# Performance work log

Measured on AMD Instinct MI355X. Metric: run time of the kernel, lower is better.

Reference implementation:

```python
import jax, jax.numpy as jnp
import numpy as np

B, S, D, H = 2, 2048, 1024, 16
HD = D // H  # head_dim = 64


def setup_inputs() -> dict:
    key = jax.random.key(0)
    ks = jax.random.split(key, 10)
    s = 1.0 / np.sqrt(D)
    # causal mask: 0 on/below diagonal, -inf above (matches masked_fill(mask == -inf))
    neg_inf = jnp.float32(-jnp.inf)
    mask = jnp.where(jnp.tril(jnp.ones((S, S), dtype=bool)), 0.0, neg_inf).astype(jnp.float32)
    return {
        "x": jax.random.normal(ks[0], (B, S, D), dtype=jnp.float32),
        "mask": mask,
        "Wq": jax.random.uniform(ks[1], (D, D), jnp.float32, -s, s),
        "bq": jax.random.uniform(ks[2], (D,), jnp.float32, -s, s),
        "Wk": jax.random.uniform(ks[3], (D, D), jnp.float32, -s, s),
        "bk": jax.random.uniform(ks[4], (D,), jnp.float32, -s, s),
        "Wv": jax.random.uniform(ks[5], (D, D), jnp.float32, -s, s),
        "bv": jax.random.uniform(ks[6], (D,), jnp.float32, -s, s),
        "Wo": jax.random.uniform(ks[7], (D, D), jnp.float32, -s, s),
        "bo": jax.random.uniform(ks[8], (D,), jnp.float32, -s, s),
    }


def reference(x, mask, Wq, bq, Wk, bk, Wv, bv, Wo, bo):
    b, s, d = x.shape
    scale = jnp.float32(HD) ** 0.5
    # qkv projections (torch Linear: y = x W^T + b), split into heads: [b, H, s, hd]
    q = (x @ Wq.T + bq).reshape(b, s, H, HD).transpose(0, 2, 1, 3)
    k = (x @ Wk.T + bk).reshape(b, s, H, HD).transpose(0, 2, 1, 3)
    v = (x @ Wv.T + bv).reshape(b, s, H, HD).transpose(0, 2, 1, 3)
    scores = jnp.einsum("bhqd,bhkd->bhqk", q, k) / scale
    scores = jnp.where(mask[None, None] == -jnp.inf, -jnp.inf, scores)
    attn = jax.nn.softmax(scores, axis=-1)
    # dropout(p=0.1) is identity in eval mode
    ctx = jnp.einsum("bhqk,bhkd->bhqd", attn, v)
    ctx = ctx.transpose(0, 2, 1, 3).reshape(b, s, d)
    return ctx @ Wo.T + bo
```

## Files before the change

### kernel.cpp

```cpp
#include <hip/hip_runtime.h>
#include <hip/hip_bf16.h>
#include <cmath>

#define S_ 2048
#define D_ 1024
#define H_ 16
#define HD_ 64
#define GM 4096
#define GN 1024
#define GK 1024
#define QSCALE 0.1803368801111f
#define THR2   11.5415603f

typedef __attribute__((ext_vector_type(4))) float f32x4;
typedef __attribute__((ext_vector_type(8))) short bf16x8;
typedef __attribute__((ext_vector_type(4))) short bf16x4;

__device__ __forceinline__ short f2bf(float f) {
    union { float f; unsigned u; } x; x.f = f;
    unsigned r = x.u + 0x7fffu + ((x.u >> 16) & 1u);
    return (short)(r >> 16);
}
__device__ __forceinline__ short bftrunc(float f) {
    union { float f; unsigned u; } x; x.f = f;
    return (short)(x.u >> 16);
}
__device__ __forceinline__ void gload16(const short* g, short* l) {
    __builtin_amdgcn_global_load_lds((const __attribute__((address_space(1))) void*)g,
                                     (__attribute__((address_space(3))) void*)l, 16, 0, 0);
}

__global__ __launch_bounds__(256) void cvt_all(
    const float* __restrict__ x,
    const float* __restrict__ w0, const float* __restrict__ w1,
    const float* __restrict__ w2, const float* __restrict__ w3,
    short* __restrict__ xb, short* __restrict__ Wb)
{
    const int bid = blockIdx.x;
    const float* src; short* dst; int loc;
    if (bid < 2048) { src = x; dst = xb; loc = bid; }
    else {
        int wsel = (bid - 2048) >> 9, wb = (bid - 2048) & 511;
        src = wsel == 0 ? w0 : wsel == 1 ? w1 : wsel == 2 ? w2 : w3;
        dst = Wb + ((size_t)wsel << 20);
        loc = wb;
    }
    int id = loc * 256 + threadIdx.x;
    const float* s = src + (size_t)id * 8;
    f32x4 a = *(const f32x4*)s;
    f32x4 b = *(const f32x4*)(s + 4);
    bf16x8 h;
    h[0] = f2bf(a[0]); h[1] = f2bf(a[1]); h[2] = f2bf(a[2]); h[3] = f2bf(a[3]);
    h[4] = f2bf(b[0]); h[5] = f2bf(b[1]); h[6] = f2bf(b[2]); h[7] = f2bf(b[3]);
    *(bf16x8*)(dst + (size_t)id * 8) = h;
}

__global__ __launch_bounds__(256) void gemm_qkv(
    const short* __restrict__ A, const short* __restrict__ W3,
    const float* __restrict__ bq, const float* __restrict__ bk, const float* __restrict__ bv,
    short* __restrict__ Qb, short* __restrict__ Kb, short* __restrict__ Vt)
{
    __shared__ short SMEM[32768];
    const int t = threadIdx.x, lane = t & 63, w = t >> 6;
    const int bid = blockIdx.x;
    const int xcd = bid & 7, idx = bid >> 3;
    const int ntile = idx % 24, mloc = idx / 24;
    const int m0 = (xcd * 4 + mloc) * 128;
    const int n0g = ntile * 128;
    const int wr = (w >> 1) * 64, wc = (w & 1) * 64;
    const int fr = lane & 15, g = lane >> 4;
    const int srow = lane >> 3;
    const int gslot = (lane & 7) ^ srow;
    const int rbase = w * 32;

    f32x4 acc[4][4] = {};

    #pragma unroll
    for (int i = 0; i < 4; ++i) {
        int row = rbase + i * 8 + srow;
        gload16(A  + (size_t)(m0 + row) * GK + gslot * 8, &SMEM[(rbase + i * 8) * 64]);
        gload16(W3 + (size_t)(n0g + row) * GK + gslot * 8, &SMEM[8192 + (rbase + i * 8) * 64]);
    }
    __syncthreads();

    int cur = 0;
    for (int t16 = 0; t16 < 16; ++t16) {
        if (t16 < 15) {
            int kt = (t16 + 1) * 64;
            short* Ad = &SMEM[(cur ^ 1) * 16384];
            short* Bd = &SMEM[(cur ^ 1) * 16384 + 8192];
            #pragma unroll
            for (int i = 0; i < 4; ++i) {
                int row = rbase + i * 8 + srow;
                gload16(A  + (size_t)(m0 + row) * GK + kt + gslot * 8, &Ad[(rbase + i * 8) * 64]);
                gload16(W3 + (size_t)(n0g + row) * GK + kt + gslot * 8, &Bd[(rbase + i * 8) * 64]);
            }
        }
        const char* Asc = (const char*)&SMEM[cur * 16384];
        const char* Bsc = (const char*)&SMEM[cur * 16384 + 8192];
        #pragma unroll
        for (int ks = 0; ks < 2; ++ks) {
            bf16x8 af[4], bf_[4];
            #pragma unroll
            for (int mb = 0; mb < 4; ++mb) {
                int row = wr + mb * 16 + fr;
                af[mb] = *(const bf16x8*)(Asc + row * 128 + (((ks * 4 + g) ^ (row & 7)) << 4));
            }
            #pragma unroll
            for (int nb = 0; nb < 4; ++nb) {
                int row = wc + nb * 16 + fr;
                bf_[nb] = *(const bf16x8*)(Bsc + row * 128 + (((ks * 4 + g) ^ (row & 7)) << 4));
            }
            #pragma unroll
            for (int mb = 0; mb < 4; ++mb)
                #pragma unroll
                for (int nb = 0; nb < 4; ++nb)
                    acc[mb][nb] = __builtin_amdgcn_mfma_f32_16x16x32_bf16(
                        af[mb], bf_[nb], acc[mb][nb], 0, 0, 0);
        }
        __syncthreads();
        cur ^= 1;
    }

    const int seg = n0g >> 10, nn = n0g & 1023;
    if (seg == 2) {
        short* Cs = SMEM;
        #pragma unroll
        for (int mb = 0; mb < 4; ++mb)
            #pragma unroll
            for (int nb = 0; nb < 4; ++nb) {
                int cl = wc + nb * 16 + fr;
                int rl_ = wr + mb * 16 + g * 4;
                float bvv = bv[nn + cl];
                bf16x4 hv;
                #pragma unroll
                for (int r = 0; r < 4; ++r) hv[r] = f2bf(acc[mb][nb][r] + bvv);
                *(bf16x4*)(Cs + cl * 136 + rl_) = hv;
            }
        __syncthreads();
        const int b = m0 >> 11;
        const int s_base = m0 & 2047;
        #pragma unroll
        for (int p = 0; p < 8; ++p) {
            int id = t + p * 256;
            int cl = id >> 4, ch = id & 15;
            int n = nn + cl;
            int h = n >> 6, d = n & 63;
            bf16x8 v = *(const bf16x8*)(Cs + cl * 136 + ch * 8);
            *(bf16x8*)(Vt + ((size_t)((b * 16 + h) * 64 + d)) * S_ + s_base + ch * 8) = v;
        }
    } else {
        const float* bp = seg ? bk : bq;
        short* dst = seg ? Kb : Qb;
        const float sc = seg ? 1.0f : QSCALE;
        #pragma unroll
        for (int mb = 0; mb < 4; ++mb)
            #pragma unroll
            for (int nb = 0; nb < 4; ++nb) {
                int grow = m0 + wr + mb * 16 + g * 4;
                int gcol = nn + wc + nb * 16 + fr;
                float bvv = bp[gcol];
                #pragma unroll
                for (int r = 0; r < 4; ++r)
                    dst[(size_t)(grow + r) * GN + gcol] = f2bf((acc[mb][nb][r] + bvv) * sc);
            }
    }
}

__global__ __launch_bounds__(256) void gemm_o(
    const short* __restrict__ A, const short* __restrict__ W,
    const float* __restrict__ bias, float* __restrict__ C)
{
    __shared__ short As[2][8192];
    __shared__ short Bs[2][4096];
    const int t = threadIdx.x, lane = t & 63, w = t >> 6;
    const int bid = blockIdx.x;
    const int xcd = bid & 7, wk = bid >> 3;
    const int m0 = (xcd * 4 + (wk & 3)) * 128;
    const int n0 = (wk >> 2) * 64;
    const int wr = (w >> 1) * 64, wc = (w & 1) * 32;
    const int fr = lane & 15, g = lane >> 4;
    const int srow = lane >> 3;
    const int gslot = (lane & 7) ^ srow;
    const int rbase = w * 32;
    const int brow = w * 16;

    f32x4 acc[4][2] = {};

    #pragma unroll
    for (int i = 0; i < 4; ++i) {
        int row = rbase + i * 8 + srow;
        gload16(A + (size_t)(m0 + row) * GK + gslot * 8, &As[0][(rbase + i * 8) * 64]);
    }
    #pragma unroll
    for (int i = 0; i < 2; ++i) {
        int row = brow + i * 8 + srow;
        gload16(W + (size_t)(n0 + row) * GK + gslot * 8, &Bs[0][(brow + i * 8) * 64]);
    }
    __syncthreads();

    int cur = 0;
    for (int t64 = 0; t64 < 16; ++t64) {
        if (t64 < 15) {
            int kt = (t64 + 1) * 64;
            #pragma unroll
            for (int i = 0; i < 4; ++i) {
                int row = rbase + i * 8 + srow;
                gload16(A + (size_t)(m0 + row) * GK + kt + gslot * 8, &As[cur ^ 1][(rbase + i * 8) * 64]);
            }
            #pragma unroll
            for (int i = 0; i < 2; ++i) {
                int row = brow + i * 8 + srow;
                gload16(W + (size_t)(n0 + row) * GK + kt + gslot * 8, &Bs[cur ^ 1][(brow + i * 8) * 64]);
            }
        }
        #pragma unroll
        for (int ks = 0; ks < 2; ++ks) {
            bf16x8 af[4], bf_[2];
            #pragma unroll
            for (int mb = 0; mb < 4; ++mb) {
                int row = wr + mb * 16 + fr;
                af[mb] = *(const bf16x8*)((const char*)&As[cur][0] + row * 128 + (((ks * 4 + g) ^ (row & 7)) << 4));
            }
            #pragma unroll
            for (int nb = 0; nb < 2; ++nb) {
                int row = wc + nb * 16 + fr;
                bf_[nb] = *(const bf16x8*)((const char*)&Bs[cur][0] + row * 128 + (((ks * 4 + g) ^ (row & 7)) << 4));
            }
            #pragma unroll
            for (int mb = 0; mb < 4; ++mb)
                #pragma unroll
                for (int nb = 0; nb < 2; ++nb)
                    acc[mb][nb] = __builtin_amdgcn_mfma_f32_16x16x32_bf16(
                        af[mb], bf_[nb], acc[mb][nb], 0, 0, 0);
        }
        __syncthreads();
        cur ^= 1;
    }

    #pragma unroll
    for (int mb = 0; mb < 4; ++mb)
        #pragma unroll
        for (int nb = 0; nb < 2; ++nb) {
            int grow = m0 + wr + mb * 16 + g * 4;
            int gcol = n0 + wc + nb * 16 + fr;
            float bvv = bias[gcol];
            #pragma unroll
            for (int r = 0; r < 4; ++r)
                C[(size_t)(grow + r) * GN + gcol] = acc[mb][nb][r] + bvv;
        }
}

__global__ __launch_bounds__(256) void attn_fwd_bf16(
    const short* __restrict__ Qb, const short* __restrict__ Kb,
    const short* __restrict__ Vtb, short* __restrict__ Ob)
{
    __shared__ short SK[2][4096];
    __shared__ short SVT[2][4096];
    __shared__ short SP[4][1024];

    const int t = threadIdx.x, lane = t & 63, w = t >> 6;
    const int g = lane >> 4, fr = lane & 15;
    const int bid = blockIdx.x;
    const int xcd = bid & 7, idx = bid >> 3;
    const int bh = xcd * 4 + (idx & 3);
    const int qt = 31 - (idx >> 2);
    const int b = bh >> 4, h = bh & 15;
    const int q0 = qt * 64;
    const int wq0 = w * 16;
    const int nt = qt + 1;

    bf16x8 qf[2];
    #pragma unroll
    for (int ks = 0; ks < 2; ++ks)
        qf[ks] = *(const bf16x8*)(Qb + (size_t)(b * S_ + q0 + wq0 + fr) * D_
                                  + h * 64 + ks * 32 + g * 8);

    const int srow8 = lane >> 3;
    const short* kp[2];
    const short* vp[2];
    short* kd0[2]; short* kd1[2]; short* vd0[2]; short* vd1[2];
    #pragma unroll
    for (int i = 0; i < 2; ++i) {
        int row = w * 16 + i * 8 + srow8;
        int gsl = (lane & 7) ^ (row & 7);
        kp[i] = Kb + (size_t)(b * S_ + row) * D_ + h * 64 + gsl * 8;
        vp[i] = Vtb + (size_t)(bh * 64 + row) * S_ + gsl * 8;
        kd0[i] = &SK[0][(w * 16 + i * 8) * 64];  kd1[i] = &SK[1][(w * 16 + i * 8) * 64];
        vd0[i] = &SVT[0][(w * 16 + i * 8) * 64]; vd1[i] = &SVT[1][(w * 16 + i * 8) * 64];
    }
    short* SPw = &SP[w][0];
    const int qsw = fr & 7;

    #pragma unroll
    for (int i = 0; i < 2; ++i) {
        gload16(kp[i], kd0[i]);
        gload16(vp[i], vd0[i]);
    }
    __syncthreads();

    f32x4 Oacc[4] = {};
    float m2 = -1e30f, lsum = 0.f;
    int cur = 0;

    for (int kt = 0; kt < nt; ++kt) {
        if (kt + 1 < nt) {
            kp[0] += 64 * D_; kp[1] += 64 * D_;
            vp[0] += 64;      vp[1] += 64;
            if (cur) {
                #pragma unroll
                for (int i = 0; i < 2; ++i) { gload16(kp[i], kd0[i]); gload16(vp[i], vd0[i]); }
            } else {
                #pragma unroll
                for (int i = 0; i < 2; ++i) { gload16(kp[i], kd1[i]); gload16(vp[i], vd1[i]); }
            }
        }
        const char* SKc = (const char*)(cur ? &SK[1][0] : &SK[0][0]);
        const char* SVc = (const char*)(cur ? &SVT[1][0] : &SVT[0][0]);

        f32x4 sacc[4] = {};
        #pragma unroll
        for (int ks = 0; ks < 2; ++ks) {
            #pragma unroll
            for (int mk = 0; mk < 4; ++mk) {
                int row = mk * 16 + fr;
                bf16x8 kf = *(const bf16x8*)(SKc + row * 128 + (((ks * 4 + g) ^ (row & 7)) << 4));
                sacc[mk] = __builtin_amdgcn_mfma_f32_16x16x32_bf16(kf, qf[ks], sacc[mk], 0, 0, 0);
            }
        }
        if (kt == qt) {
            #pragma unroll
            for (int mk = 0; mk < 4; ++mk)
                #pragma unroll
                for (int r = 0; r < 4; ++r)
                    if (mk * 16 + g * 4 + r > wq0 + fr) sacc[mk][r] = -1e30f;
        }

        float mx[4];
        #pragma unroll
        for (int mk = 0; mk < 4; ++mk)
            mx[mk] = fmaxf(fmaxf(sacc[mk][0], sacc[mk][1]), fmaxf(sacc[mk][2], sacc[mk][3]));
        float rm = fmaxf(fmaxf(mx[0], mx[1]), fmaxf(mx[2], mx[3]));
        rm = fmaxf(rm, __shfl_xor(rm, 16));
        rm = fmaxf(rm, __shfl_xor(rm, 32));
        if (rm > m2 + THR2) {
            float resc = exp2f(m2 - rm);
            m2 = rm;
            lsum *= resc;
            #pragma unroll
            for (int md = 0; md < 4; ++md)
                #pragma unroll
                for (int r = 0; r < 4; ++r) Oacc[md][r] *= resc;
        }
        float psk[4];
        #pragma unroll
        for (int mk = 0; mk < 4; ++mk) {
            float p0 = exp2f(sacc[mk][0] - m2);
            float p1 = exp2f(sacc[mk][1] - m2);
            float p2 = exp2f(sacc[mk][2] - m2);
            float p3 = exp2f(sacc[mk][3] - m2);
            psk[mk] = (p0 + p1) + (p2 + p3);
            bf16x4 pk;
            pk[0] = bftrunc(p0); pk[1] = bftrunc(p1);
            pk[2] = bftrunc(p2); pk[3] = bftrunc(p3);
            int k = mk * 16 + g * 4;
            *(bf16x4*)((char*)SPw + fr * 128 + (((k >> 3) ^ qsw) << 4) + ((k & 7) << 1)) = pk;
        }
        float ps = (psk[0] + psk[1]) + (psk[2] + psk[3]);
        ps += __shfl_xor(ps, 16);
        ps += __shfl_xor(ps, 32);
        lsum += ps;

        #pragma unroll
        for (int ks = 0; ks < 2; ++ks) {
            bf16x8 pf = *(const bf16x8*)((const char*)SPw + fr * 128 + (((ks * 4 + g) ^ qsw) << 4));
            #pragma unroll
            for (int md = 0; md < 4; ++md) {
                int row = md * 16 + fr;
                bf16x8 vf = *(const bf16x8*)(SVc + row * 128 + (((ks * 4 + g) ^ (row & 7)) << 4));
                Oacc[md] = __builtin_amdgcn_mfma_f32_16x16x32_bf16(vf, pf, Oacc[md], 0, 0, 0);
            }
        }
        __syncthreads();
        cur ^= 1;
    }

    const float rl = 1.f / lsum;
    const size_t orow = (size_t)(b * S_ + q0 + wq0 + fr) * D_ + h * 64;
    #pragma unroll
    for (int md = 0; md < 4; ++md) {
        bf16x4 ov;
        #pragma unroll
        for (int r = 0; r < 4; ++r) ov[r] = f2bf(Oacc[md][r] * rl);
        *(bf16x4*)(Ob + orow + md * 16 + g * 4) = ov;
    }
}

extern "C" void kernel_launch(void* const* d_in, const int* in_sizes, int n_in,
                              void* d_out, int out_size, void* d_ws, size_t ws_size,
                              hipStream_t stream)
{
    const float* x  = (const float*)d_in[0];
    const float* Wq = (const float*)d_in[2];
    const float* bq = (const float*)d_in[3];
    const float* Wk = (const float*)d_in[4];
    const float* bk = (const float*)d_in[5];
    const float* Wv = (const float*)d_in[6];
    const float* bv = (const float*)d_in[7];
    const float* Wo = (const float*)d_in[8];
    const float* bo = (const float*)d_in[9];
    float* out = (float*)d_out;

    const size_t MD = (size_t)GM * D_;
    short* xb = (short*)d_ws;
    short* Wb = xb + MD;
    short* Qb = Wb + 4 * (size_t)D_ * D_;
    short* Kb = Qb + MD;
    short* Vt = Kb + MD;
    short* Ob = Vt + MD;

    dim3 blk(256);
    cvt_all<<<dim3(4096), blk, 0, stream>>>(x, Wq, Wk, Wv, Wo, xb, Wb);
    gemm_qkv<<<dim3(768), blk, 0, stream>>>(xb, Wb, bq, bk, bv, Qb, Kb, Vt);
    attn_fwd_bf16<<<dim3(1024), blk, 0, stream>>>(Qb, Kb, Vt, Ob);
    gemm_o<<<dim3(512), blk, 0, stream>>>(Ob, Wb + 3 * (size_t)D_ * D_, bo, out);
}
```

Measured before the change: 113.3 us.

## Use two warps per attention block, each handling 32 query rows

```diff
diff --git a/kernel.cpp b/kernel.cpp
--- a/kernel.cpp
+++ b/kernel.cpp
@@ -251,13 +251,13 @@
         }
 }
 
-__global__ __launch_bounds__(256) void attn_fwd_bf16(
+__global__ __launch_bounds__(128) void attn_fwd_bf16(
     const short* __restrict__ Qb, const short* __restrict__ Kb,
     const short* __restrict__ Vtb, short* __restrict__ Ob)
 {
     __shared__ short SK[2][4096];
     __shared__ short SVT[2][4096];
-    __shared__ short SP[4][1024];
+    __shared__ short SP[2][2048];
 
     const int t = threadIdx.x, lane = t & 63, w = t >> 6;
     const int g = lane >> 4, fr = lane & 15;
@@ -267,132 +267,163 @@
     const int qt = 31 - (idx >> 2);
     const int b = bh >> 4, h = bh & 15;
     const int q0 = qt * 64;
-    const int wq0 = w * 16;
+    const int wq0 = w * 32;
     const int nt = qt + 1;
 
-    bf16x8 qf[2];
-    #pragma unroll
-    for (int ks = 0; ks < 2; ++ks)
-        qf[ks] = *(const bf16x8*)(Qb + (size_t)(b * S_ + q0 + wq0 + fr) * D_
-                                  + h * 64 + ks * 32 + g * 8);
+    bf16x8 qf[2][2];
+    #pragma unroll
+    for (int nq = 0; nq < 2; ++nq)
+        #pragma unroll
+        for (int ks = 0; ks < 2; ++ks)
+            qf[nq][ks] = *(const bf16x8*)(Qb + (size_t)(b * S_ + q0 + wq0 + nq * 16 + fr) * D_
+                                          + h * 64 + ks * 32 + g * 8);
 
     const int srow8 = lane >> 3;
-    const short* kp[2];
-    const short* vp[2];
-    short* kd0[2]; short* kd1[2]; short* vd0[2]; short* vd1[2];
-    #pragma unroll
-    for (int i = 0; i < 2; ++i) {
-        int row = w * 16 + i * 8 + srow8;
+    const short* kp[4];
+    const short* vp[4];
+    short* kd0[4]; short* kd1[4]; short* vd0[4]; short* vd1[4];
+    #pragma unroll
+    for (int i = 0; i < 4; ++i) {
+        int row = w * 32 + i * 8 + srow8;
         int gsl = (lane & 7) ^ (row & 7);
         kp[i] = Kb + (size_t)(b * S_ + row) * D_ + h * 64 + gsl * 8;
         vp[i] = Vtb + (size_t)(bh * 64 + row) * S_ + gsl * 8;
-        kd0[i] = &SK[0][(w * 16 + i * 8) * 64];  kd1[i] = &SK[1][(w * 16 + i * 8) * 64];
-        vd0[i] = &SVT[0][(w * 16 + i * 8) * 64]; vd1[i] = &SVT[1][(w * 16 + i * 8) * 64];
+        kd0[i] = &SK[0][(w * 32 + i * 8) * 64];  kd1[i] = &SK[1][(w * 32 + i * 8) * 64];
+        vd0[i] = &SVT[0][(w * 32 + i * 8) * 64]; vd1[i] = &SVT[1][(w * 32 + i * 8) * 64];
     }
     short* SPw = &SP[w][0];
     const int qsw = fr & 7;
 
     #pragma unroll
-    for (int i = 0; i < 2; ++i) {
+    for (int i = 0; i < 4; ++i) {
         gload16(kp[i], kd0[i]);
         gload16(vp[i], vd0[i]);
     }
     __syncthreads();
 
-    f32x4 Oacc[4] = {};
-    float m2 = -1e30f, lsum = 0.f;
+    f32x4 Oacc[2][4] = {};
+    float m2[2] = { -1e30f, -1e30f };
+    float lsum[2] = { 0.f, 0.f };
     int cur = 0;
 
     for (int kt = 0; kt < nt; ++kt) {
         if (kt + 1 < nt) {
-            kp[0] += 64 * D_; kp[1] += 64 * D_;
-            vp[0] += 64;      vp[1] += 64;
+            #pragma unroll
+            for (int i = 0; i < 4; ++i) { kp[i] += 64 * D_; vp[i] += 64; }
             if (cur) {
                 #pragma unroll
-                for (int i = 0; i < 2; ++i) { gload16(kp[i], kd0[i]); gload16(vp[i], vd0[i]); }
+                for (int i = 0; i < 4; ++i) { gload16(kp[i], kd0[i]); gload16(vp[i], vd0[i]); }
             } else {
                 #pragma unroll
-                for (int i = 0; i < 2; ++i) { gload16(kp[i], kd1[i]); gload16(vp[i], vd1[i]); }
+                for (int i = 0; i < 4; ++i) { gload16(kp[i], kd1[i]); gload16(vp[i], vd1[i]); }
             }
         }
         const char* SKc = (const char*)(cur ? &SK[1][0] : &SK[0][0]);
         const char* SVc = (const char*)(cur ? &SVT[1][0] : &SVT[0][0]);
 
-        f32x4 sacc[4] = {};
-        #pragma unroll
-        for (int ks = 0; ks < 2; ++ks) {
+        bf16x8 kf[2][4];
+        #pragma unroll
+        for (int ks = 0; ks < 2; ++ks)
             #pragma unroll
             for (int mk = 0; mk < 4; ++mk) {
                 int row = mk * 16 + fr;
-                bf16x8 kf = *(const bf16x8*)(SKc + row * 128 + (((ks * 4 + g) ^ (row & 7)) << 4));
-                sacc[mk] = __builtin_amdgcn_mfma_f32_16x16x32_bf16(kf, qf[ks], sacc[mk], 0, 0, 0);
-            }
-        }
+                kf[ks][mk] = *(const bf16x8*)(SKc + row * 128 + (((ks * 4 + g) ^ (row & 7)) << 4));
+            }
+
+        f32x4 sacc[2][4] = {};
+        #pragma unroll
+        for (int nq = 0; nq < 2; ++nq)
+            #pragma unroll
+            for (int ks = 0; ks < 2; ++ks)
+                #pragma unroll
+                for (int mk = 0; mk < 4; ++mk)
+                    sacc[nq][mk] = __builtin_amdgcn_mfma_f32_16x16x32_bf16(
+                        kf[ks][mk], qf[nq][ks], sacc[nq][mk], 0, 0, 0);
+
         if (kt == qt) {
             #pragma unroll
-            for (int mk = 0; mk < 4; ++mk)
-                #pragma unroll
-                for (int r = 0; r < 4; ++r)
-                    if (mk * 16 + g * 4 + r > wq0 + fr) sacc[mk][r] = -1e30f;
-        }
-
-        float mx[4];
-        #pragma unroll
-        for (int mk = 0; mk < 4; ++mk)
-            mx[mk] = fmaxf(fmaxf(sacc[mk][0], sacc[mk][1]), fmaxf(sacc[mk][2], sacc[mk][3]));
-        float rm = fmaxf(fmaxf(mx[0], mx[1]), fmaxf(mx[2], mx[3]));
-        rm = fmaxf(rm, __shfl_xor(rm, 16));
-        rm = fmaxf(rm, __shfl_xor(rm, 32));
-        if (rm > m2 + THR2) {
-            float resc = exp2f(m2 - rm);
-            m2 = rm;
-            lsum *= resc;
-            #pragma unroll
-            for (int md = 0; md < 4; ++md)
-                #pragma unroll
-                for (int r = 0; r < 4; ++r) Oacc[md][r] *= resc;
-        }
-        float psk[4];
-        #pragma unroll
-        for (int mk = 0; mk < 4; ++mk) {
-            float p0 = exp2f(sacc[mk][0] - m2);
-            float p1 = exp2f(sacc[mk][1] - m2);
-            float p2 = exp2f(sacc[mk][2] - m2);
-            float p3 = exp2f(sacc[mk][3] - m2);
-            psk[mk] = (p0 + p1) + (p2 + p3);
-            bf16x4 pk;
-            pk[0] = bftrunc(p0); pk[1] = bftrunc(p1);
-            pk[2] = bftrunc(p2); pk[3] = bftrunc(p3);
-            int k = mk * 16 + g * 4;
-            *(bf16x4*)((char*)SPw + fr * 128 + (((k >> 3) ^ qsw) << 4) + ((k & 7) << 1)) = pk;
-        }
-        float ps = (psk[0] + psk[1]) + (psk[2] + psk[3]);
-        ps += __shfl_xor(ps, 16);
-        ps += __shfl_xor(ps, 32);
-        lsum += ps;
+            for (int nq = 0; nq < 2; ++nq) {
+                int ql = wq0 + nq * 16 + fr;
+                #pragma unroll
+                for (int mk = 0; mk < 4; ++mk)
+                    #pragma unroll
+                    for (int r = 0; r < 4; ++r)
+                        if (mk * 16 + g * 4 + r > ql) sacc[nq][mk][r] = -1e30f;
+            }
+        }
+
+        #pragma unroll
+        for (int nq = 0; nq < 2; ++nq) {
+            float mx0 = fmaxf(fmaxf(sacc[nq][0][0], sacc[nq][0][1]), fmaxf(sacc[nq][0][2], sacc[nq][0][3]));
+            float mx1 = fmaxf(fmaxf(sacc[nq][1][0], sacc[nq][1][1]), fmaxf(sacc[nq][1][2], sacc[nq][1][3]));
+            float mx2 = fmaxf(fmaxf(sacc[nq][2][0], sacc[nq][2][1]), fmaxf(sacc[nq][2][2], sacc[nq][2][3]));
+            float mx3 = fmaxf(fmaxf(sacc[nq][3][0], sacc[nq][3][1]), fmaxf(sacc[nq][3][2], sacc[nq][3][3]));
+            float rm = fmaxf(fmaxf(mx0, mx1), fmaxf(mx2, mx3));
+            rm = fmaxf(rm, __shfl_xor(rm, 16));
+            rm = fmaxf(rm, __shfl_xor(rm, 32));
+            if (rm > m2[nq] + THR2) {
+                float resc = exp2f(m2[nq] - rm);
+                m2[nq] = rm;
+                lsum[nq] *= resc;
+                #pragma unroll
+                for (int md = 0; md < 4; ++md)
+                    #pragma unroll
+                    for (int r = 0; r < 4; ++r) Oacc[nq][md][r] *= resc;
+            }
+            const int qlr = nq * 16 + fr;
+            float psk[4];
+            #pragma unroll
+            for (int mk = 0; mk < 4; ++mk) {
+                float p0 = exp2f(sacc[nq][mk][0] - m2[nq]);
+                float p1 = exp2f(sacc[nq][mk][1] - m2[nq]);
+                float p2 = exp2f(sacc[nq][mk][2] - m2[nq]);
+                float p3 = exp2f(sacc[nq][mk][3] - m2[nq]);
+                psk[mk] = (p0 + p1) + (p2 + p3);
+                bf16x4 pk;
+                pk[0] = bftrunc(p0); pk[1] = bftrunc(p1);
+                pk[2] = bftrunc(p2); pk[3] = bftrunc(p3);
+                int k = mk * 16 + g * 4;
+                *(bf16x4*)((char*)SPw + qlr * 128 + (((k >> 3) ^ qsw) << 4) + ((k & 7) << 1)) = pk;
+            }
+            float ps = (psk[0] + psk[1]) + (psk[2] + psk[3]);
+            ps += __shfl_xor(ps, 16);
+            ps += __shfl_xor(ps, 32);
+            lsum[nq] += ps;
+        }
 
         #pragma unroll
         for (int ks = 0; ks < 2; ++ks) {
-            bf16x8 pf = *(const bf16x8*)((const char*)SPw + fr * 128 + (((ks * 4 + g) ^ qsw) << 4));
+            bf16x8 vf[4];
             #pragma unroll
             for (int md = 0; md < 4; ++md) {
                 int row = md * 16 + fr;
-                bf16x8 vf = *(const bf16x8*)(SVc + row * 128 + (((ks * 4 + g) ^ (row & 7)) << 4));
-                Oacc[md] = __builtin_amdgcn_mfma_f32_16x16x32_bf16(vf, pf, Oacc[md], 0, 0, 0);
+                vf[md] = *(const bf16x8*)(SVc + row * 128 + (((ks * 4 + g) ^ (row & 7)) << 4));
+            }
+            #pragma unroll
+            for (int nq = 0; nq < 2; ++nq) {
+                int qlr = nq * 16 + fr;
+                bf16x8 pf = *(const bf16x8*)((const char*)SPw + qlr * 128 + (((ks * 4 + g) ^ qsw) << 4));
+                #pragma unroll
+                for (int md = 0; md < 4; ++md)
+                    Oacc[nq][md] = __builtin_amdgcn_mfma_f32_16x16x32_bf16(
+                        vf[md], pf, Oacc[nq][md], 0, 0, 0);
             }
         }
         __syncthreads();
         cur ^= 1;
     }
 
-    const float rl = 1.f / lsum;
-    const size_t orow = (size_t)(b * S_ + q0 + wq0 + fr) * D_ + h * 64;
-    #pragma unroll
-    for (int md = 0; md < 4; ++md) {
-        bf16x4 ov;
-        #pragma unroll
-        for (int r = 0; r < 4; ++r) ov[r] = f2bf(Oacc[md][r] * rl);
-        *(bf16x4*)(Ob + orow + md * 16 + g * 4) = ov;
+    #pragma unroll
+    for (int nq = 0; nq < 2; ++nq) {
+        const float rl = 1.f / lsum[nq];
+        const size_t orow = (size_t)(b * S_ + q0 + wq0 + nq * 16 + fr) * D_ + h * 64;
+        #pragma unroll
+        for (int md = 0; md < 4; ++md) {
+            bf16x4 ov;
+            #pragma unroll
+            for (int r = 0; r < 4; ++r) ov[r] = f2bf(Oacc[nq][md][r] * rl);
+            *(bf16x4*)(Ob + orow + md * 16 + g * 4) = ov;
+        }
     }
 }
 
@@ -422,6 +453,6 @@
     dim3 blk(256);
     cvt_all<<<dim3(4096), blk, 0, stream>>>(x, Wq, Wk, Wv, Wo, xb, Wb);
     gemm_qkv<<<dim3(768), blk, 0, stream>>>(xb, Wb, bq, bk, bv, Qb, Kb, Vt);
-    attn_fwd_bf16<<<dim3(1024), blk, 0, stream>>>(Qb, Kb, Vt, Ob);
+    attn_fwd_bf16<<<dim3(1024), dim3(128), 0, stream>>>(Qb, Kb, Vt, Ob);
     gemm_o<<<dim3(512), blk, 0, stream>>>(Ob, Wb + 3 * (size_t)D_ * D_, bo, out);
 }
```

Measured after the change: 128.4 us. 13.4% more time.
